# Optimization experiments

Measured on AMD Instinct MI355X. Metric: run time of the kernel, lower is better.

The kernel has to match this reference:

```python
import jax, jax.numpy as jnp
import numpy as np

TEMPERATURE = 0.5
NEG_FILL = -9000000000000000.0


def setup_inputs() -> dict:
    key = jax.random.key(0)
    k1, k2 = jax.random.split(key)
    z1 = jax.random.normal(k1, (4096, 256), dtype=jnp.float32)
    z2 = jax.random.normal(k2, (4096, 256), dtype=jnp.float32)
    return {"z1": z1, "z2": z2}


def reference(z1, z2):
    N = z1.shape[0]
    z = jnp.concatenate([z1, z2], axis=0)  # [2N, d]
    # cosine similarity: normalize once (eps matches torch's 1e-8) then GEMM
    norm = jnp.maximum(jnp.linalg.norm(z, axis=-1, keepdims=True), 1e-8)
    zn = z / norm
    sim = (zn @ zn.T) / TEMPERATURE  # [2N, 2N]
    # mask out self-similarity on the diagonal
    diag = jnp.eye(2 * N, dtype=bool)
    sim = jnp.where(diag, NEG_FILL, sim)
    labels = jnp.concatenate([jnp.arange(N) + N, jnp.arange(N)])  # positive pairs
    logp = jax.nn.log_softmax(sim, axis=-1)
    loss = -jnp.mean(jnp.take_along_axis(logp, labels[:, None], axis=1))
    return loss
```

## Files before the change

kernel.cpp:

```cpp
#include <hip/hip_runtime.h>
#include <hip/hip_bf16.h>


#define TWO_N 8192
#define NPAIR 4096
#define DDIM  256
#define NT    64
#define NBLK  (NT * (NT + 1) / 2)
#define INV_T 2.0f
#define GEMM_GRID 512

typedef __attribute__((ext_vector_type(8))) short bf16x8;
typedef __attribute__((ext_vector_type(4))) float f32x4;

typedef __attribute__((address_space(1))) void gvoid_t;
typedef __attribute__((address_space(3))) void lvoid_t;

__device__ __forceinline__ void gload_lds16(const void* g, void* l) {
    __builtin_amdgcn_global_load_lds((gvoid_t*)g, (lvoid_t*)l, 16, 0, 0);
}

__global__ void k_normalize(const float* __restrict__ z1,
                            const float* __restrict__ z2,
                            __hip_bfloat16* __restrict__ zn,
                            float* __restrict__ e_diag,
                            float* __restrict__ pos,
                            float* __restrict__ row_sumexp,
                            float* __restrict__ out) {
    if (threadIdx.x < 8) row_sumexp[blockIdx.x * 8 + threadIdx.x] = 0.0f;
    if (blockIdx.x == 0 && threadIdx.x == 0) out[0] = 0.0f;

    const int w    = threadIdx.x >> 6;
    const int lane = threadIdx.x & 63;
    const int i    = blockIdx.x * 4 + w;

    float4 a = ((const float4*)(z1 + (size_t)i * DDIM))[lane];
    float4 b = ((const float4*)(z2 + (size_t)i * DDIM))[lane];

    float s1 = a.x * a.x + a.y * a.y + a.z * a.z + a.w * a.w;
    float s2 = b.x * b.x + b.y * b.y + b.z * b.z + b.w * b.w;
    float dd = a.x * b.x + a.y * b.y + a.z * b.z + a.w * b.w;
#pragma unroll
    for (int m = 1; m < 64; m <<= 1) {
        s1 += __shfl_xor(s1, m, 64);
        s2 += __shfl_xor(s2, m, 64);
        dd += __shfl_xor(dd, m, 64);
    }

    float inv1 = 1.0f / fmaxf(sqrtf(s1), 1e-8f);
    float inv2 = 1.0f / fmaxf(sqrtf(s2), 1e-8f);

    __hip_bfloat16 q1[4], q2[4];
    q1[0] = __float2bfloat16(a.x * inv1); q1[1] = __float2bfloat16(a.y * inv1);
    q1[2] = __float2bfloat16(a.z * inv1); q1[3] = __float2bfloat16(a.w * inv1);
    q2[0] = __float2bfloat16(b.x * inv2); q2[1] = __float2bfloat16(b.y * inv2);
    q2[2] = __float2bfloat16(b.z * inv2); q2[3] = __float2bfloat16(b.w * inv2);

    float qs1 = 0.0f, qs2 = 0.0f;
#pragma unroll
    for (int j = 0; j < 4; ++j) {
        float f1 = __bfloat162float(q1[j]);
        float f2 = __bfloat162float(q2[j]);
        qs1 += f1 * f1;
        qs2 += f2 * f2;
    }
#pragma unroll
    for (int m = 1; m < 64; m <<= 1) {
        qs1 += __shfl_xor(qs1, m, 64);
        qs2 += __shfl_xor(qs2, m, 64);
    }

    *reinterpret_cast<uint2*>(zn + (size_t)i * DDIM + lane * 4) =
        *reinterpret_cast<uint2*>(q1);
    *reinterpret_cast<uint2*>(zn + (size_t)(i + NPAIR) * DDIM + lane * 4) =
        *reinterpret_cast<uint2*>(q2);

    if (lane == 0) {
        e_diag[i]         = __expf(qs1 * INV_T);
        e_diag[i + NPAIR] = __expf(qs2 * INV_T);
        pos[i]            = dd * inv1 * inv2 * INV_T;
    }
}

__global__ __launch_bounds__(512, 2)
void k_gemm_sumexp(const __hip_bfloat16* __restrict__ zn,
                   float* __restrict__ row_sumexp) {
    __shared__ __align__(128) __hip_bfloat16 Asmem[128 * DDIM];

    const int tid  = threadIdx.x;
    const int lane = tid & 63;
    const int w    = tid >> 6;
    const int wr   = w >> 2;
    const int wc   = w & 3;
    const int lr   = lane & 15;
    const int quad = lane >> 4;

    const int t0 = (int)(((long)blockIdx.x * NBLK) >> 9);
    const int t1 = (int)(((long)(blockIdx.x + 1) * NBLK) >> 9);

    int b = t0;
    int rt = (int)(64.5f - sqrtf(64.5f * 64.5f - 2.0f * (float)b));
    if (rt < 0) rt = 0;
    if (rt > NT - 1) rt = NT - 1;
    while (rt > 0 && NT * rt - (rt * (rt - 1)) / 2 > b) --rt;
    while (NT * (rt + 1) - ((rt + 1) * rt) / 2 <= b) ++rt;
    int ct = rt + (b - (NT * rt - (rt * (rt - 1)) / 2));

    int pa[4];
#pragma unroll
    for (int mi = 0; mi < 4; ++mi)
        pa[mi] = (wr * 64 + mi * 16 + lr) * (DDIM * 2) + ((quad ^ (lr & 7)) << 4);

    int cur_rt = -1;
    f32x4 acc[4][2];
    float rs[4][4];
#pragma unroll
    for (int mi = 0; mi < 4; ++mi)
#pragma unroll
        for (int r = 0; r < 4; ++r) rs[mi][r] = 0.0f;
    int  pCol = 0;
    bool pDiag = false, havePrev = false;

    auto epi_accum = [&](float& cs0, float& cs1) {
#pragma unroll
        for (int mi = 0; mi < 4; ++mi)
#pragma unroll
            for (int r = 0; r < 4; ++r) {
                float e0 = __expf(acc[mi][0][r] * INV_T);
                float e1 = __expf(acc[mi][1][r] * INV_T);
                rs[mi][r] += e0 + e1;
                cs0 += e0;
                cs1 += e1;
            }
    };
    auto epi_cols = [&](float cs0, float cs1) {
        if (pDiag) { cs0 = 0.0f; cs1 = 0.0f; }
        cs0 += __shfl_xor(cs0, 16, 64); cs0 += __shfl_xor(cs0, 32, 64);
        cs1 += __shfl_xor(cs1, 16, 64); cs1 += __shfl_xor(cs1, 32, 64);
        if (quad == 0) {
            atomicAdd(&row_sumexp[pCol + wc * 32 + lr], cs0);
            atomicAdd(&row_sumexp[pCol + wc * 32 + 16 + lr], cs1);
        }
    };
    auto flush_rows = [&](int rowb) {
#pragma unroll
        for (int mi = 0; mi < 4; ++mi)
#pragma unroll
            for (int r = 0; r < 4; ++r) {
                float v = rs[mi][r];
                v += __shfl_xor(v, 1, 64);
                v += __shfl_xor(v, 2, 64);
                v += __shfl_xor(v, 4, 64);
                v += __shfl_xor(v, 8, 64);
                if (lr == 0)
                    atomicAdd(&row_sumexp[rowb + wr * 64 + mi * 16 + quad * 4 + r], v);
                rs[mi][r] = 0.0f;
            }
    };

    for (int t = t0; t < t1; ++t) {
        const int  row_base = rt * 128;
        const int  col_base = ct * 128;
        const bool diag     = (rt == ct);
        const bool restage  = (rt != cur_rt);

        const __hip_bfloat16* gB0 =
            zn + (size_t)(col_base + wc * 32 + lr) * DDIM + quad * 8;
        bf16x8 Bfr[8][2];

        if (restage) {
            if (havePrev) { float c0 = 0.f, c1 = 0.f; epi_accum(c0, c1); epi_cols(c0, c1); }
            if (cur_rt >= 0) flush_rows(cur_rt * 128);
            __syncthreads();
            const int ck = (tid & 24) | ((tid & 7) ^ ((tid >> 5) & 7));
            const char* gA = (const char*)(zn + (size_t)row_base * DDIM)
                           + (tid >> 5) * (DDIM * 2) + ck * 16;
            char* lA = (char*)Asmem + tid * 16;
#pragma unroll
            for (int j = 0; j < 8; ++j)
                gload_lds16(gA + (size_t)j * 16 * (DDIM * 2), lA + j * 8192);
#pragma unroll
            for (int ks = 0; ks < 8; ++ks) {
                const __hip_bfloat16* p0 = gB0 + ks * 32;
                const __hip_bfloat16* p1 = p0 + 16 * DDIM;
                asm volatile("global_load_dwordx4 %0, %1, off"
                             : "=v"(Bfr[ks][0]) : "v"(p0) : "memory");
                asm volatile("global_load_dwordx4 %0, %1, off"
                             : "=v"(Bfr[ks][1]) : "v"(p1) : "memory");
            }
            cur_rt = rt;
            asm volatile("s_waitcnt vmcnt(0)" ::: "memory");
            __syncthreads();
        } else {
#pragma unroll
            for (int ks = 0; ks < 4; ++ks) {
                const __hip_bfloat16* p0 = gB0 + ks * 32;
                const __hip_bfloat16* p1 = p0 + 16 * DDIM;
                asm volatile("global_load_dwordx4 %0, %1, off"
                             : "=v"(Bfr[ks][0]) : "v"(p0) : "memory");
                asm volatile("global_load_dwordx4 %0, %1, off"
                             : "=v"(Bfr[ks][1]) : "v"(p1) : "memory");
            }
            float c0 = 0.f, c1 = 0.f;
            epi_accum(c0, c1);
#pragma unroll
            for (int ks = 4; ks < 8; ++ks) {
                const __hip_bfloat16* p0 = gB0 + ks * 32;
                const __hip_bfloat16* p1 = p0 + 16 * DDIM;
                asm volatile("global_load_dwordx4 %0, %1, off"
                             : "=v"(Bfr[ks][0]) : "v"(p0) : "memory");
                asm volatile("global_load_dwordx4 %0, %1, off"
                             : "=v"(Bfr[ks][1]) : "v"(p1) : "memory");
            }
            epi_cols(c0, c1);
            asm volatile("s_waitcnt vmcnt(2)" ::: "memory");
        }
        __builtin_amdgcn_sched_barrier(0);

        pCol = col_base; pDiag = diag; havePrev = true;

#pragma unroll
        for (int mi = 0; mi < 4; ++mi)
#pragma unroll
            for (int ni = 0; ni < 2; ++ni)
                acc[mi][ni] = (f32x4){0.f, 0.f, 0.f, 0.f};

        bf16x8 afc[4];
#pragma unroll
        for (int mi = 0; mi < 4; ++mi)
            afc[mi] = *(const bf16x8*)((const char*)Asmem + pa[mi]);

#pragma unroll
        for (int kstep = 0; kstep < 8; ++kstep) {
            bf16x8 afn[4];
            if (kstep < 7) {
                const int kn   = kstep + 1;
                const int koff = (kn >> 1) << 7;
                const int kx   = (kn & 1) << 6;
#pragma unroll
                for (int mi = 0; mi < 4; ++mi)
                    afn[mi] = *(const bf16x8*)((const char*)Asmem + ((pa[mi] ^ kx) + koff));
            }
#pragma unroll
            for (int mi = 0; mi < 4; ++mi)
#pragma unroll
                for (int ni = 0; ni < 2; ++ni)
                    acc[mi][ni] = __builtin_amdgcn_mfma_f32_16x16x32_bf16(
                        afc[mi], Bfr[kstep][ni], acc[mi][ni], 0, 0, 0);
            if (kstep < 7) {
#pragma unroll
                for (int mi = 0; mi < 4; ++mi) afc[mi] = afn[mi];
            }
        }

        if (++ct >= NT) { ++rt; ct = rt; }
    }

    { float c0 = 0.f, c1 = 0.f; epi_accum(c0, c1); epi_cols(c0, c1); }
    flush_rows(cur_rt * 128);
}

__global__ void k_final(const float* __restrict__ row_sumexp,
                        const float* __restrict__ e_diag,
                        const float* __restrict__ pos,
                        float* __restrict__ out) {
    const int i    = blockIdx.x * 256 + threadIdx.x;
    const int w    = threadIdx.x >> 6;
    const int lane = threadIdx.x & 63;

    float t = logf(row_sumexp[i] - e_diag[i])
            + logf(row_sumexp[i + NPAIR] - e_diag[i + NPAIR])
            - 2.0f * pos[i];
#pragma unroll
    for (int m = 1; m < 64; m <<= 1) t += __shfl_xor(t, m, 64);

    __shared__ float ps[4];
    if (lane == 0) ps[w] = t;
    __syncthreads();
    if (threadIdx.x == 0) {
        float s = (ps[0] + ps[1] + ps[2] + ps[3]) * (1.0f / (float)TWO_N);
        atomicAdd(out, s);
    }
}

extern "C" void kernel_launch(void* const* d_in, const int* in_sizes, int n_in,
                              void* d_out, int out_size, void* d_ws, size_t ws_size,
                              hipStream_t stream) {
    const float* z1 = (const float*)d_in[0];
    const float* z2 = (const float*)d_in[1];
    float* out = (float*)d_out;

    char* ws = (char*)d_ws;
    __hip_bfloat16* zn  = (__hip_bfloat16*)ws;
    float* row_sumexp   = (float*)(ws + (size_t)TWO_N * DDIM * 2);
    float* e_diag       = row_sumexp + TWO_N;
    float* pos          = e_diag + TWO_N;

    k_normalize<<<NPAIR / 4, 256, 0, stream>>>(z1, z2, zn, e_diag, pos,
                                               row_sumexp, out);
    k_gemm_sumexp<<<GEMM_GRID, 512, 0, stream>>>(zn, row_sumexp);
    k_final<<<NPAIR / 256, 256, 0, stream>>>(row_sumexp, e_diag, pos, out);
}
```

Measured before the change: 132.0 us.

## Fuse normalize, GEMM-sumexp and final reduction into one persistent kernel

Merges the normalize, GEMM/sum-exp and final-loss kernels into one kernel. A global atomic spin barrier separates the normalize phase from the GEMM phase, and a last-block-done counter runs the final reduction. The grid is halved to 256 blocks so every block can be co-resident, which the spin barrier needs, and each block handles twice as many tiles. This removes launch gaps and an extra kernel but adds a grid barrier, and it risks deadlock or load imbalance if not all blocks fit on the device at once.

```diff
diff --git a/kernel.cpp b/kernel.cpp
--- a/kernel.cpp
+++ b/kernel.cpp
@@ -8,7 +8,7 @@
 #define NT    64
 #define NBLK  (NT * (NT + 1) / 2)
 #define INV_T 2.0f
-#define GEMM_GRID 512
+#define GEMM_GRID 256
 
 typedef __attribute__((ext_vector_type(8))) short bf16x8;
 typedef __attribute__((ext_vector_type(4))) float f32x4;
@@ -20,266 +20,289 @@
     __builtin_amdgcn_global_load_lds((gvoid_t*)g, (lvoid_t*)l, 16, 0, 0);
 }
 
-__global__ void k_normalize(const float* __restrict__ z1,
-                            const float* __restrict__ z2,
-                            __hip_bfloat16* __restrict__ zn,
-                            float* __restrict__ e_diag,
-                            float* __restrict__ pos,
-                            float* __restrict__ row_sumexp,
-                            float* __restrict__ out) {
-    if (threadIdx.x < 8) row_sumexp[blockIdx.x * 8 + threadIdx.x] = 0.0f;
-    if (blockIdx.x == 0 && threadIdx.x == 0) out[0] = 0.0f;
-
-    const int w    = threadIdx.x >> 6;
-    const int lane = threadIdx.x & 63;
-    const int i    = blockIdx.x * 4 + w;
-
-    float4 a = ((const float4*)(z1 + (size_t)i * DDIM))[lane];
-    float4 b = ((const float4*)(z2 + (size_t)i * DDIM))[lane];
-
-    float s1 = a.x * a.x + a.y * a.y + a.z * a.z + a.w * a.w;
-    float s2 = b.x * b.x + b.y * b.y + b.z * b.z + b.w * b.w;
-    float dd = a.x * b.x + a.y * b.y + a.z * b.z + a.w * b.w;
-#pragma unroll
-    for (int m = 1; m < 64; m <<= 1) {
-        s1 += __shfl_xor(s1, m, 64);
-        s2 += __shfl_xor(s2, m, 64);
-        dd += __shfl_xor(dd, m, 64);
-    }
-
-    float inv1 = 1.0f / fmaxf(sqrtf(s1), 1e-8f);
-    float inv2 = 1.0f / fmaxf(sqrtf(s2), 1e-8f);
-
-    __hip_bfloat16 q1[4], q2[4];
-    q1[0] = __float2bfloat16(a.x * inv1); q1[1] = __float2bfloat16(a.y * inv1);
-    q1[2] = __float2bfloat16(a.z * inv1); q1[3] = __float2bfloat16(a.w * inv1);
-    q2[0] = __float2bfloat16(b.x * inv2); q2[1] = __float2bfloat16(b.y * inv2);
-    q2[2] = __float2bfloat16(b.z * inv2); q2[3] = __float2bfloat16(b.w * inv2);
-
-    float qs1 = 0.0f, qs2 = 0.0f;
-#pragma unroll
-    for (int j = 0; j < 4; ++j) {
-        float f1 = __bfloat162float(q1[j]);
-        float f2 = __bfloat162float(q2[j]);
-        qs1 += f1 * f1;
-        qs2 += f2 * f2;
-    }
-#pragma unroll
-    for (int m = 1; m < 64; m <<= 1) {
-        qs1 += __shfl_xor(qs1, m, 64);
-        qs2 += __shfl_xor(qs2, m, 64);
-    }
-
-    *reinterpret_cast<uint2*>(zn + (size_t)i * DDIM + lane * 4) =
-        *reinterpret_cast<uint2*>(q1);
-    *reinterpret_cast<uint2*>(zn + (size_t)(i + NPAIR) * DDIM + lane * 4) =
-        *reinterpret_cast<uint2*>(q2);
-
-    if (lane == 0) {
-        e_diag[i]         = __expf(qs1 * INV_T);
-        e_diag[i + NPAIR] = __expf(qs2 * INV_T);
-        pos[i]            = dd * inv1 * inv2 * INV_T;
-    }
+__global__ void k_zero(float* __restrict__ out, unsigned* __restrict__ bar) {
+    if (threadIdx.x == 0) { out[0] = 0.0f; bar[0] = 0u; bar[1] = 0u; }
 }
 
 __global__ __launch_bounds__(512, 2)
-void k_gemm_sumexp(const __hip_bfloat16* __restrict__ zn,
-                   float* __restrict__ row_sumexp) {
+void k_fused(const float* __restrict__ z1,
+             const float* __restrict__ z2,
+             __hip_bfloat16* __restrict__ zn,
+             float* __restrict__ e_diag,
+             float* __restrict__ pos,
+             float* __restrict__ row_sumexp,
+             float* __restrict__ out,
+             unsigned* __restrict__ bar) {
     __shared__ __align__(128) __hip_bfloat16 Asmem[128 * DDIM];
+    __shared__ unsigned lastFlag;
+    __shared__ float ps[8];
 
     const int tid  = threadIdx.x;
     const int lane = tid & 63;
     const int w    = tid >> 6;
-    const int wr   = w >> 2;
-    const int wc   = w & 3;
-    const int lr   = lane & 15;
-    const int quad = lane >> 4;
-
-    const int t0 = (int)(((long)blockIdx.x * NBLK) >> 9);
-    const int t1 = (int)(((long)(blockIdx.x + 1) * NBLK) >> 9);
-
-    int b = t0;
-    int rt = (int)(64.5f - sqrtf(64.5f * 64.5f - 2.0f * (float)b));
-    if (rt < 0) rt = 0;
-    if (rt > NT - 1) rt = NT - 1;
-    while (rt > 0 && NT * rt - (rt * (rt - 1)) / 2 > b) --rt;
-    while (NT * (rt + 1) - ((rt + 1) * rt) / 2 <= b) ++rt;
-    int ct = rt + (b - (NT * rt - (rt * (rt - 1)) / 2));
-
-    int pa[4];
-#pragma unroll
-    for (int mi = 0; mi < 4; ++mi)
-        pa[mi] = (wr * 64 + mi * 16 + lr) * (DDIM * 2) + ((quad ^ (lr & 7)) << 4);
-
-    int cur_rt = -1;
-    f32x4 acc[4][2];
-    float rs[4][4];
-#pragma unroll
-    for (int mi = 0; mi < 4; ++mi)
-#pragma unroll
-        for (int r = 0; r < 4; ++r) rs[mi][r] = 0.0f;
-    int  pCol = 0;
-    bool pDiag = false, havePrev = false;
-
-    auto epi_accum = [&](float& cs0, float& cs1) {
+
+    {
+        if (tid < 32) row_sumexp[blockIdx.x * 32 + tid] = 0.0f;
+
+#pragma unroll
+        for (int rep = 0; rep < 2; ++rep) {
+            const int i = blockIdx.x * 16 + rep * 8 + w;
+
+            float4 a = ((const float4*)(z1 + (size_t)i * DDIM))[lane];
+            float4 b = ((const float4*)(z2 + (size_t)i * DDIM))[lane];
+
+            float s1 = a.x * a.x + a.y * a.y + a.z * a.z + a.w * a.w;
+            float s2 = b.x * b.x + b.y * b.y + b.z * b.z + b.w * b.w;
+            float dd = a.x * b.x + a.y * b.y + a.z * b.z + a.w * b.w;
+#pragma unroll
+            for (int m = 1; m < 64; m <<= 1) {
+                s1 += __shfl_xor(s1, m, 64);
+                s2 += __shfl_xor(s2, m, 64);
+                dd += __shfl_xor(dd, m, 64);
+            }
+
+            float inv1 = 1.0f / fmaxf(sqrtf(s1), 1e-8f);
+            float inv2 = 1.0f / fmaxf(sqrtf(s2), 1e-8f);
+
+            __hip_bfloat16 q1[4], q2[4];
+            q1[0] = __float2bfloat16(a.x * inv1); q1[1] = __float2bfloat16(a.y * inv1);
+            q1[2] = __float2bfloat16(a.z * inv1); q1[3] = __float2bfloat16(a.w * inv1);
+            q2[0] = __float2bfloat16(b.x * inv2); q2[1] = __float2bfloat16(b.y * inv2);
+            q2[2] = __float2bfloat16(b.z * inv2); q2[3] = __float2bfloat16(b.w * inv2);
+
+            float qs1 = 0.0f, qs2 = 0.0f;
+#pragma unroll
+            for (int j = 0; j < 4; ++j) {
+                float f1 = __bfloat162float(q1[j]);
+                float f2 = __bfloat162float(q2[j]);
+                qs1 += f1 * f1;
+                qs2 += f2 * f2;
+            }
+#pragma unroll
+            for (int m = 1; m < 64; m <<= 1) {
+                qs1 += __shfl_xor(qs1, m, 64);
+                qs2 += __shfl_xor(qs2, m, 64);
+            }
+
+            *reinterpret_cast<uint2*>(zn + (size_t)i * DDIM + lane * 4) =
+                *reinterpret_cast<uint2*>(q1);
+            *reinterpret_cast<uint2*>(zn + (size_t)(i + NPAIR) * DDIM + lane * 4) =
+                *reinterpret_cast<uint2*>(q2);
+
+            if (lane == 0) {
+                e_diag[i]         = __expf(qs1 * INV_T);
+                e_diag[i + NPAIR] = __expf(qs2 * INV_T);
+                pos[i]            = dd * inv1 * inv2 * INV_T;
+            }
+        }
+    }
+
+    __syncthreads();
+    if (tid == 0) {
+        __threadfence();
+        atomicAdd(&bar[0], 1u);
+        while (atomicAdd(&bar[0], 0u) < (unsigned)GEMM_GRID)
+            __builtin_amdgcn_s_sleep(2);
+        __threadfence();
+    }
+    __syncthreads();
+
+    {
+        const int wr   = w >> 2;
+        const int wc   = w & 3;
+        const int lr   = lane & 15;
+        const int quad = lane >> 4;
+
+        const int t0 = (int)(((long)blockIdx.x * NBLK) >> 8);
+        const int t1 = (int)(((long)(blockIdx.x + 1) * NBLK) >> 8);
+
+        int b = t0;
+        int rt = (int)(64.5f - sqrtf(64.5f * 64.5f - 2.0f * (float)b));
+        if (rt < 0) rt = 0;
+        if (rt > NT - 1) rt = NT - 1;
+        while (rt > 0 && NT * rt - (rt * (rt - 1)) / 2 > b) --rt;
+        while (NT * (rt + 1) - ((rt + 1) * rt) / 2 <= b) ++rt;
+        int ct = rt + (b - (NT * rt - (rt * (rt - 1)) / 2));
+
+        int pa[4];
 #pragma unroll
         for (int mi = 0; mi < 4; ++mi)
-#pragma unroll
-            for (int r = 0; r < 4; ++r) {
-                float e0 = __expf(acc[mi][0][r] * INV_T);
-                float e1 = __expf(acc[mi][1][r] * INV_T);
-                rs[mi][r] += e0 + e1;
-                cs0 += e0;
-                cs1 += e1;
-            }
-    };
-    auto epi_cols = [&](float cs0, float cs1) {
-        if (pDiag) { cs0 = 0.0f; cs1 = 0.0f; }
-        cs0 += __shfl_xor(cs0, 16, 64); cs0 += __shfl_xor(cs0, 32, 64);
-        cs1 += __shfl_xor(cs1, 16, 64); cs1 += __shfl_xor(cs1, 32, 64);
-        if (quad == 0) {
-            atomicAdd(&row_sumexp[pCol + wc * 32 + lr], cs0);
-            atomicAdd(&row_sumexp[pCol + wc * 32 + 16 + lr], cs1);
+            pa[mi] = (wr * 64 + mi * 16 + lr) * (DDIM * 2) + ((quad ^ (lr & 7)) << 4);
+
+        int cur_rt = -1;
+        f32x4 acc[4][2];
+        float rs[4][4];
+#pragma unroll
+        for (int mi = 0; mi < 4; ++mi)
+#pragma unroll
+            for (int r = 0; r < 4; ++r) rs[mi][r] = 0.0f;
+        int  pCol = 0;
+        bool pDiag = false, havePrev = false;
+
+        auto epi_accum = [&](float& cs0, float& cs1) {
+#pragma unroll
+            for (int mi = 0; mi < 4; ++mi)
+#pragma unroll
+                for (int r = 0; r < 4; ++r) {
+                    float e0 = __expf(acc[mi][0][r] * INV_T);
+                    float e1 = __expf(acc[mi][1][r] * INV_T);
+                    rs[mi][r] += e0 + e1;
+                    cs0 += e0;
+                    cs1 += e1;
+                }
+        };
+        auto epi_cols = [&](float cs0, float cs1) {
+            if (pDiag) { cs0 = 0.0f; cs1 = 0.0f; }
+            cs0 += __shfl_xor(cs0, 16, 64); cs0 += __shfl_xor(cs0, 32, 64);
+            cs1 += __shfl_xor(cs1, 16, 64); cs1 += __shfl_xor(cs1, 32, 64);
+            if (quad == 0) {
+                atomicAdd(&row_sumexp[pCol + wc * 32 + lr], cs0);
+                atomicAdd(&row_sumexp[pCol + wc * 32 + 16 + lr], cs1);
+            }
+        };
+        auto flush_rows = [&](int rowb) {
+#pragma unroll
+            for (int mi = 0; mi < 4; ++mi)
+#pragma unroll
+                for (int r = 0; r < 4; ++r) {
+                    float v = rs[mi][r];
+                    v += __shfl_xor(v, 1, 64);
+                    v += __shfl_xor(v, 2, 64);
+                    v += __shfl_xor(v, 4, 64);
+                    v += __shfl_xor(v, 8, 64);
+                    if (lr == 0)
+                        atomicAdd(&row_sumexp[rowb + wr * 64 + mi * 16 + quad * 4 + r], v);
+                    rs[mi][r] = 0.0f;
+                }
+        };
+
+        for (int t = t0; t < t1; ++t) {
+            const int  row_base = rt * 128;
+            const int  col_base = ct * 128;
+            const bool diag     = (rt == ct);
+            const bool restage  = (rt != cur_rt);
+
+            const __hip_bfloat16* gB0 =
+                zn + (size_t)(col_base + wc * 32 + lr) * DDIM + quad * 8;
+            bf16x8 Bfr[8][2];
+
+            if (restage) {
+                if (havePrev) { float c0 = 0.f, c1 = 0.f; epi_accum(c0, c1); epi_cols(c0, c1); }
+                if (cur_rt >= 0) flush_rows(cur_rt * 128);
+                __syncthreads();
+                const int ck = (tid & 24) | ((tid & 7) ^ ((tid >> 5) & 7));
+                const char* gA = (const char*)(zn + (size_t)row_base * DDIM)
+                               + (tid >> 5) * (DDIM * 2) + ck * 16;
+                char* lA = (char*)Asmem + tid * 16;
+#pragma unroll
+                for (int j = 0; j < 8; ++j)
+                    gload_lds16(gA + (size_t)j * 16 * (DDIM * 2), lA + j * 8192);
+#pragma unroll
+                for (int ks = 0; ks < 8; ++ks) {
+                    const __hip_bfloat16* p0 = gB0 + ks * 32;
+                    const __hip_bfloat16* p1 = p0 + 16 * DDIM;
+                    asm volatile("global_load_dwordx4 %0, %1, off"
+                                 : "=v"(Bfr[ks][0]) : "v"(p0) : "memory");
+                    asm volatile("global_load_dwordx4 %0, %1, off"
+                                 : "=v"(Bfr[ks][1]) : "v"(p1) : "memory");
+                }
+                cur_rt = rt;
+                asm volatile("s_waitcnt vmcnt(0)" ::: "memory");
+                __syncthreads();
+            } else {
+#pragma unroll
+                for (int ks = 0; ks < 4; ++ks) {
+                    const __hip_bfloat16* p0 = gB0 + ks * 32;
+                    const __hip_bfloat16* p1 = p0 + 16 * DDIM;
+                    asm volatile("global_load_dwordx4 %0, %1, off"
+                                 : "=v"(Bfr[ks][0]) : "v"(p0) : "memory");
+                    asm volatile("global_load_dwordx4 %0, %1, off"
+                                 : "=v"(Bfr[ks][1]) : "v"(p1) : "memory");
+                }
+                float c0 = 0.f, c1 = 0.f;
+                epi_accum(c0, c1);
+#pragma unroll
+                for (int ks = 4; ks < 8; ++ks) {
+                    const __hip_bfloat16* p0 = gB0 + ks * 32;
+                    const __hip_bfloat16* p1 = p0 + 16 * DDIM;
+                    asm volatile("global_load_dwordx4 %0, %1, off"
+                                 : "=v"(Bfr[ks][0]) : "v"(p0) : "memory");
+                    asm volatile("global_load_dwordx4 %0, %1, off"
+                                 : "=v"(Bfr[ks][1]) : "v"(p1) : "memory");
+                }
+                epi_cols(c0, c1);
+                asm volatile("s_waitcnt vmcnt(2)" ::: "memory");
+            }
+            __builtin_amdgcn_sched_barrier(0);
+
+            pCol = col_base; pDiag = diag; havePrev = true;
+
+#pragma unroll
+            for (int mi = 0; mi < 4; ++mi)
+#pragma unroll
+                for (int ni = 0; ni < 2; ++ni)
+                    acc[mi][ni] = (f32x4){0.f, 0.f, 0.f, 0.f};
+
+            bf16x8 afc[4];
+#pragma unroll
+            for (int mi = 0; mi < 4; ++mi)
+                afc[mi] = *(const bf16x8*)((const char*)Asmem + pa[mi]);
+
+#pragma unroll
+            for (int kstep = 0; kstep < 8; ++kstep) {
+                bf16x8 afn[4];
+                if (kstep < 7) {
+                    const int kn   = kstep + 1;
+                    const int koff = (kn >> 1) << 7;
+                    const int kx   = (kn & 1) << 6;
+#pragma unroll
+                    for (int mi = 0; mi < 4; ++mi)
+                        afn[mi] = *(const bf16x8*)((const char*)Asmem + ((pa[mi] ^ kx) + koff));
+                }
+#pragma unroll
+                for (int mi = 0; mi < 4; ++mi)
+#pragma unroll
+                    for (int ni = 0; ni < 2; ++ni)
+                        acc[mi][ni] = __builtin_amdgcn_mfma_f32_16x16x32_bf16(
+                            afc[mi], Bfr[kstep][ni], acc[mi][ni], 0, 0, 0);
+                if (kstep < 7) {
+#pragma unroll
+                    for (int mi = 0; mi < 4; ++mi) afc[mi] = afn[mi];
+                }
+            }
+
+            if (++ct >= NT) { ++rt; ct = rt; }
         }
-    };
-    auto flush_rows = [&](int rowb) {
-#pragma unroll
-        for (int mi = 0; mi < 4; ++mi)
-#pragma unroll
-            for (int r = 0; r < 4; ++r) {
-                float v = rs[mi][r];
-                v += __shfl_xor(v, 1, 64);
-                v += __shfl_xor(v, 2, 64);
-                v += __shfl_xor(v, 4, 64);
-                v += __shfl_xor(v, 8, 64);
-                if (lr == 0)
-                    atomicAdd(&row_sumexp[rowb + wr * 64 + mi * 16 + quad * 4 + r], v);
-                rs[mi][r] = 0.0f;
-            }
-    };
-
-    for (int t = t0; t < t1; ++t) {
-        const int  row_base = rt * 128;
-        const int  col_base = ct * 128;
-        const bool diag     = (rt == ct);
-        const bool restage  = (rt != cur_rt);
-
-        const __hip_bfloat16* gB0 =
-            zn + (size_t)(col_base + wc * 32 + lr) * DDIM + quad * 8;
-        bf16x8 Bfr[8][2];
-
-        if (restage) {
-            if (havePrev) { float c0 = 0.f, c1 = 0.f; epi_accum(c0, c1); epi_cols(c0, c1); }
-            if (cur_rt >= 0) flush_rows(cur_rt * 128);
-            __syncthreads();
-            const int ck = (tid & 24) | ((tid & 7) ^ ((tid >> 5) & 7));
-            const char* gA = (const char*)(zn + (size_t)row_base * DDIM)
-                           + (tid >> 5) * (DDIM * 2) + ck * 16;
-            char* lA = (char*)Asmem + tid * 16;
-#pragma unroll
-            for (int j = 0; j < 8; ++j)
-                gload_lds16(gA + (size_t)j * 16 * (DDIM * 2), lA + j * 8192);
-#pragma unroll
-            for (int ks = 0; ks < 8; ++ks) {
-                const __hip_bfloat16* p0 = gB0 + ks * 32;
-                const __hip_bfloat16* p1 = p0 + 16 * DDIM;
-                asm volatile("global_load_dwordx4 %0, %1, off"
-                             : "=v"(Bfr[ks][0]) : "v"(p0) : "memory");
-                asm volatile("global_load_dwordx4 %0, %1, off"
-                             : "=v"(Bfr[ks][1]) : "v"(p1) : "memory");
-            }
-            cur_rt = rt;
-            asm volatile("s_waitcnt vmcnt(0)" ::: "memory");
-            __syncthreads();
-        } else {
-#pragma unroll
-            for (int ks = 0; ks < 4; ++ks) {
-                const __hip_bfloat16* p0 = gB0 + ks * 32;
-                const __hip_bfloat16* p1 = p0 + 16 * DDIM;
-                asm volatile("global_load_dwordx4 %0, %1, off"
-                             : "=v"(Bfr[ks][0]) : "v"(p0) : "memory");
-                asm volatile("global_load_dwordx4 %0, %1, off"
-                             : "=v"(Bfr[ks][1]) : "v"(p1) : "memory");
-            }
-            float c0 = 0.f, c1 = 0.f;
-            epi_accum(c0, c1);
-#pragma unroll
-            for (int ks = 4; ks < 8; ++ks) {
-                const __hip_bfloat16* p0 = gB0 + ks * 32;
-                const __hip_bfloat16* p1 = p0 + 16 * DDIM;
-                asm volatile("global_load_dwordx4 %0, %1, off"
-                             : "=v"(Bfr[ks][0]) : "v"(p0) : "memory");
-                asm volatile("global_load_dwordx4 %0, %1, off"
-                             : "=v"(Bfr[ks][1]) : "v"(p1) : "memory");
-            }
-            epi_cols(c0, c1);
-            asm volatile("s_waitcnt vmcnt(2)" ::: "memory");
+
+        { float c0 = 0.f, c1 = 0.f; epi_accum(c0, c1); epi_cols(c0, c1); }
+        flush_rows(cur_rt * 128);
+    }
+
+    __syncthreads();
+    if (tid == 0) {
+        __threadfence();
+        unsigned prev = atomicAdd(&bar[1], 1u);
+        lastFlag = (prev == (unsigned)(GEMM_GRID - 1)) ? 1u : 0u;
+    }
+    __syncthreads();
+
+    if (lastFlag) {
+        float t = 0.0f;
+        for (int p = tid; p < NPAIR; p += 512) {
+            t += logf(row_sumexp[p] - e_diag[p])
+               + logf(row_sumexp[p + NPAIR] - e_diag[p + NPAIR])
+               - 2.0f * pos[p];
         }
-        __builtin_amdgcn_sched_barrier(0);
-
-        pCol = col_base; pDiag = diag; havePrev = true;
-
-#pragma unroll
-        for (int mi = 0; mi < 4; ++mi)
-#pragma unroll
-            for (int ni = 0; ni < 2; ++ni)
-                acc[mi][ni] = (f32x4){0.f, 0.f, 0.f, 0.f};
-
-        bf16x8 afc[4];
-#pragma unroll
-        for (int mi = 0; mi < 4; ++mi)
-            afc[mi] = *(const bf16x8*)((const char*)Asmem + pa[mi]);
-
-#pragma unroll
-        for (int kstep = 0; kstep < 8; ++kstep) {
-            bf16x8 afn[4];
-            if (kstep < 7) {
-                const int kn   = kstep + 1;
-                const int koff = (kn >> 1) << 7;
-                const int kx   = (kn & 1) << 6;
-#pragma unroll
-                for (int mi = 0; mi < 4; ++mi)
-                    afn[mi] = *(const bf16x8*)((const char*)Asmem + ((pa[mi] ^ kx) + koff));
-            }
-#pragma unroll
-            for (int mi = 0; mi < 4; ++mi)
-#pragma unroll
-                for (int ni = 0; ni < 2; ++ni)
-                    acc[mi][ni] = __builtin_amdgcn_mfma_f32_16x16x32_bf16(
-                        afc[mi], Bfr[kstep][ni], acc[mi][ni], 0, 0, 0);
-            if (kstep < 7) {
-#pragma unroll
-                for (int mi = 0; mi < 4; ++mi) afc[mi] = afn[mi];
-            }
+#pragma unroll
+        for (int m = 1; m < 64; m <<= 1) t += __shfl_xor(t, m, 64);
+        if (lane == 0) ps[w] = t;
+        __syncthreads();
+        if (tid == 0) {
+            float s = 0.0f;
+#pragma unroll
+            for (int j = 0; j < 8; ++j) s += ps[j];
+            out[0] = s * (1.0f / (float)TWO_N);
         }
-
-        if (++ct >= NT) { ++rt; ct = rt; }
-    }
-
-    { float c0 = 0.f, c1 = 0.f; epi_accum(c0, c1); epi_cols(c0, c1); }
-    flush_rows(cur_rt * 128);
-}
-
-__global__ void k_final(const float* __restrict__ row_sumexp,
-                        const float* __restrict__ e_diag,
-                        const float* __restrict__ pos,
-                        float* __restrict__ out) {
-    const int i    = blockIdx.x * 256 + threadIdx.x;
-    const int w    = threadIdx.x >> 6;
-    const int lane = threadIdx.x & 63;
-
-    float t = logf(row_sumexp[i] - e_diag[i])
-            + logf(row_sumexp[i + NPAIR] - e_diag[i + NPAIR])
-            - 2.0f * pos[i];
-#pragma unroll
-    for (int m = 1; m < 64; m <<= 1) t += __shfl_xor(t, m, 64);
-
-    __shared__ float ps[4];
-    if (lane == 0) ps[w] = t;
-    __syncthreads();
-    if (threadIdx.x == 0) {
-        float s = (ps[0] + ps[1] + ps[2] + ps[3]) * (1.0f / (float)TWO_N);
-        atomicAdd(out, s);
     }
 }
 
@@ -295,9 +318,9 @@
     float* row_sumexp   = (float*)(ws + (size_t)TWO_N * DDIM * 2);
     float* e_diag       = row_sumexp + TWO_N;
     float* pos          = e_diag + TWO_N;
-
-    k_normalize<<<NPAIR / 4, 256, 0, stream>>>(z1, z2, zn, e_diag, pos,
-                                               row_sumexp, out);
-    k_gemm_sumexp<<<GEMM_GRID, 512, 0, stream>>>(zn, row_sumexp);
-    k_final<<<NPAIR / 256, 256, 0, stream>>>(row_sumexp, e_diag, pos, out);
+    unsigned* bar       = (unsigned*)(pos + NPAIR);
+
+    k_zero<<<1, 64, 0, stream>>>(out, bar);
+    k_fused<<<GEMM_GRID, 512, 0, stream>>>(z1, z2, zn, e_diag, pos,
+                                           row_sumexp, out, bar);
 }
```

Measured after the change: 141.3 us. 7.0% more time.
